# Performance work log

Measured on AMD Instinct MI355X. Metric: run time of the kernel, lower is better.

Reference implementation:

```python
import jax, jax.numpy as jnp
import numpy as np

N, E, G = 100000, 1600000, 1024
F_IN, D, C = 1, 32, 10

def _lin(key, fin, fout):
    return jax.random.normal(key, (fin, fout), jnp.float32) / np.sqrt(fin)

def setup_inputs() -> dict:
    key = jax.random.key(0)
    ks = jax.random.split(key, 32)
    inp = {}
    inp['x'] = jax.random.normal(ks[0], (N, F_IN), jnp.float32)
    inp['edge_index'] = jax.random.randint(ks[1], (2, E), 0, N)
    inp['batch'] = jnp.sort(jax.random.randint(ks[2], (N,), 0, G))
    inp['num_graphs'] = G
    # conv1: ResGatedGraphConv(F_IN -> D)
    inp['c1_Wk'] = _lin(ks[3], F_IN, D); inp['c1_bk'] = jnp.zeros((D,), jnp.float32)
    inp['c1_Wq'] = _lin(ks[4], F_IN, D); inp['c1_bq'] = jnp.zeros((D,), jnp.float32)
    inp['c1_Wv'] = _lin(ks[5], F_IN, D); inp['c1_bv'] = jnp.zeros((D,), jnp.float32)
    inp['c1_Wskip'] = _lin(ks[6], F_IN, D); inp['c1_b'] = jnp.zeros((D,), jnp.float32)
    # conv2: FiLMConv(D -> D), num_relations=1
    inp['c2_Wlin'] = _lin(ks[7], D, D)
    inp['c2_Wfilm'] = _lin(ks[8], D, 2 * D); inp['c2_bfilm'] = jnp.zeros((2 * D,), jnp.float32)
    inp['c2_Wls'] = _lin(ks[9], D, D)
    inp['c2_Wfs'] = _lin(ks[10], D, 2 * D)
    # conv3: ResGatedGraphConv(D -> D)
    inp['c3_Wk'] = _lin(ks[11], D, D); inp['c3_bk'] = jnp.zeros((D,), jnp.float32)
    inp['c3_Wq'] = _lin(ks[12], D, D); inp['c3_bq'] = jnp.zeros((D,), jnp.float32)
    inp['c3_Wv'] = _lin(ks[13], D, D); inp['c3_bv'] = jnp.zeros((D,), jnp.float32)
    inp['c3_Wskip'] = _lin(ks[14], D, D); inp['c3_b'] = jnp.zeros((D,), jnp.float32)
    # final classifier
    inp['lin_W'] = _lin(ks[15], D, C); inp['lin_b'] = jnp.zeros((C,), jnp.float32)
    return inp

def _res_gated(x, src, dst, Wk, bk, Wq, bq, Wv, bv, Wskip, b):
    # out_i = sum_{j->i} sigmoid(k_i + q_j) * v_j + W_skip x_i + b
    k = x @ Wk + bk
    q = x @ Wq + bq
    v = x @ Wv + bv
    msg = jax.nn.sigmoid(k[dst] + q[src]) * v[src]  # [E, D]
    agg = jax.ops.segment_sum(msg, dst, num_segments=x.shape[0])
    return agg + x @ Wskip + b

def _film(x, src, dst, Wlin, Wfilm, bfilm, Wls, Wfs):
    # skip path: relu(gamma_skip * (W_skip x) + beta_skip)
    bg_s = x @ Wfs                       # [N, 2D]
    beta_s, gamma_s = jnp.split(bg_s, 2, axis=-1)
    out = jax.nn.relu(gamma_s * (x @ Wls) + beta_s)
    # message path: relu(gamma_i * (W x_j) + beta_i), mean aggregation
    bg = x @ Wfilm + bfilm
    beta, gamma = jnp.split(bg, 2, axis=-1)
    xl = x @ Wlin
    msg = jax.nn.relu(gamma[dst] * xl[src] + beta[dst])  # [E, D]
    sums = jax.ops.segment_sum(msg, dst, num_segments=x.shape[0])
    cnt = jax.ops.segment_sum(jnp.ones((dst.shape[0], 1), x.dtype), dst, num_segments=x.shape[0])
    return out + sums / jnp.maximum(cnt, 1.0)

def reference(x, edge_index, batch, num_graphs,
              c1_Wk, c1_bk, c1_Wq, c1_bq, c1_Wv, c1_bv, c1_Wskip, c1_b,
              c2_Wlin, c2_Wfilm, c2_bfilm, c2_Wls, c2_Wfs,
              c3_Wk, c3_bk, c3_Wq, c3_bq, c3_Wv, c3_bv, c3_Wskip, c3_b,
              lin_W, lin_b):
    src, dst = edge_index[0], edge_index[1]
    h = _res_gated(x, src, dst, c1_Wk, c1_bk, c1_Wq, c1_bq, c1_Wv, c1_bv, c1_Wskip, c1_b)
    h = jax.nn.relu(h)
    h = _film(h, src, dst, c2_Wlin, c2_Wfilm, c2_bfilm, c2_Wls, c2_Wfs)
    h = jax.nn.relu(h)
    h = _res_gated(h, src, dst, c3_Wk, c3_bk, c3_Wq, c3_bq, c3_Wv, c3_bv, c3_Wskip, c3_b)
    # global mean pool over graphs
    sums = jax.ops.segment_sum(h, batch, num_segments=num_graphs)
    cnt = jax.ops.segment_sum(jnp.ones((h.shape[0], 1), h.dtype), batch, num_segments=num_graphs)
    g = sums / jnp.maximum(cnt, 1.0)
    # dropout is identity in eval mode
    return g @ lin_W + lin_b
```

## Files before the change

### kernel.cpp

```cpp
#include <hip/hip_runtime.h>

#define N_NODES 100000
#define N_EDGES 1600000
#define N_GRAPH 1024
#define NB      196
#define BCAP    10240
#define PEPT    16

typedef unsigned short u16;
typedef unsigned int   u32;

__device__ __forceinline__ u16 f2bf(float f) {
    u32 u = __float_as_uint(f);
    u += 0x7FFFu + ((u >> 16) & 1u);
    return (u16)(u >> 16);
}
__device__ __forceinline__ float bf2f(u16 h) { return __uint_as_float(((u32)h) << 16); }
__device__ __forceinline__ float rcpf(float x) { return __builtin_amdgcn_rcpf(x); }

__global__ __launch_bounds__(256) void k_partition(const int* __restrict__ ei,
                                                   int* __restrict__ gcnt,
                                                   int* __restrict__ bucketed)
{
    __shared__ int lcnt[NB], gbase[NB], lcur[NB];
    int t = threadIdx.x;
    for (int i = t; i < NB; i += 256) { lcnt[i] = 0; lcur[i] = 0; }
    __syncthreads();

    int ebase = blockIdx.x * (256 * PEPT);
    int pk[PEPT], bk[PEPT];
#pragma unroll
    for (int r = 0; r < PEPT; r++) {
        int e = ebase + r * 256 + t;
        if (e < N_EDGES) {
            int d = ei[N_EDGES + e];
            int s = ei[e];
            int b = d >> 9;
            bk[r] = b;
            pk[r] = ((d & 511) << 17) | s;
            atomicAdd(&lcnt[b], 1);
        } else bk[r] = -1;
    }
    __syncthreads();
    for (int i = t; i < NB; i += 256) gbase[i] = atomicAdd(&gcnt[i], lcnt[i]);
    __syncthreads();
#pragma unroll
    for (int r = 0; r < PEPT; r++) {
        if (bk[r] >= 0) {
            int b = bk[r];
            int pos = gbase[b] + atomicAdd(&lcur[b], 1);
            bucketed[b * BCAP + pos] = pk[r];
        }
    }
}

__global__ __launch_bounds__(512) void k_place(const int* __restrict__ bucketed,
                                               const int* __restrict__ gcnt,
                                               int* __restrict__ csr,
                                               int* __restrict__ starts,
                                               int* __restrict__ cnt)
{
    __shared__ int sb[256];
    __shared__ int scnt[512], sexc[512], scur[512];
    int b = blockIdx.x, t = threadIdx.x;

    if (t < 256) sb[t] = (t < NB) ? gcnt[t] : 0;
    __syncthreads();
#pragma unroll
    for (int off = 1; off < 256; off <<= 1) {
        int u = 0;
        if (t < 256 && t >= off) u = sb[t - off];
        __syncthreads();
        if (t < 256) sb[t] += u;
        __syncthreads();
    }
    int ecnt = gcnt[b];
    int ebase = sb[b] - ecnt;
    const int* bp = bucketed + b * BCAP;

    scnt[t] = 0; scur[t] = 0;
    __syncthreads();
    for (int e = t; e < ecnt; e += 512) atomicAdd(&scnt[bp[e] >> 17], 1);
    __syncthreads();
    int v = scnt[t];
    sexc[t] = v;
    __syncthreads();
#pragma unroll
    for (int off = 1; off < 512; off <<= 1) {
        int u = (t >= off) ? sexc[t - off] : 0;
        __syncthreads();
        sexc[t] += u;
        __syncthreads();
    }
    int excl = sexc[t] - v;
    __syncthreads();
    sexc[t] = excl;
    __syncthreads();

    int node = b * 512 + t;
    if (node < N_NODES) { starts[node] = ebase + excl; cnt[node] = v; }

    for (int e = t; e < ecnt; e += 512) {
        int p = bp[e];
        int ld = p >> 17;
        int pos = ebase + sexc[ld] + atomicAdd(&scur[ld], 1);
        csr[pos] = p & 0x1FFFF;
    }
}

#define EDGE1(XS, ACC) {                                                     \
    ACC.x += fmaf(XS, wv.x, bv4.x) *                                         \
             rcpf(fmaf(ek.x, __expf(-fmaf(XS, wq.x, bq4.x)), 1.0f));         \
    ACC.y += fmaf(XS, wv.y, bv4.y) *                                         \
             rcpf(fmaf(ek.y, __expf(-fmaf(XS, wq.y, bq4.y)), 1.0f));         \
    ACC.z += fmaf(XS, wv.z, bv4.z) *                                         \
             rcpf(fmaf(ek.z, __expf(-fmaf(XS, wq.z, bq4.z)), 1.0f));         \
    ACC.w += fmaf(XS, wv.w, bv4.w) *                                         \
             rcpf(fmaf(ek.w, __expf(-fmaf(XS, wq.w, bq4.w)), 1.0f)); }

__global__ __launch_bounds__(256) void k_gath1(
    const float* __restrict__ x, const int* __restrict__ csr_src,
    const int* __restrict__ starts, const int* __restrict__ cnt,
    const float* __restrict__ Wk, const float* __restrict__ bk,
    const float* __restrict__ Wq, const float* __restrict__ bq,
    const float* __restrict__ Wv, const float* __restrict__ bv,
    const float* __restrict__ Wskip, const float* __restrict__ b,
    u16* __restrict__ h1b)
{
    int tid = blockIdx.x * 256 + threadIdx.x;
    int i = tid >> 3, l = tid & 7;

    float xd = x[i];
    float4 wk = ((const float4*)Wk)[l], bk4 = ((const float4*)bk)[l];
    float4 wq = ((const float4*)Wq)[l], bq4 = ((const float4*)bq)[l];
    float4 wv = ((const float4*)Wv)[l], bv4 = ((const float4*)bv)[l];
    float4 ek;
    ek.x = __expf(-fmaf(xd, wk.x, bk4.x));
    ek.y = __expf(-fmaf(xd, wk.y, bk4.y));
    ek.z = __expf(-fmaf(xd, wk.z, bk4.z));
    ek.w = __expf(-fmaf(xd, wk.w, bk4.w));

    int base = starts[i], deg = cnt[i];
    float4 a0 = make_float4(0.f, 0.f, 0.f, 0.f);
    float4 a1 = make_float4(0.f, 0.f, 0.f, 0.f);
    int e = 0;
    for (; e + 3 < deg; e += 4) {
        int s0 = csr_src[base + e];
        int s1 = csr_src[base + e + 1];
        int s2 = csr_src[base + e + 2];
        int s3 = csr_src[base + e + 3];
        float x0 = x[s0], x1 = x[s1], x2 = x[s2], x3 = x[s3];
        EDGE1(x0, a0) EDGE1(x1, a1) EDGE1(x2, a0) EDGE1(x3, a1)
    }
    for (; e < deg; e++) {
        float x0 = x[csr_src[base + e]];
        EDGE1(x0, a0)
    }
    float4 ws4 = ((const float4*)Wskip)[l];
    float4 bb4 = ((const float4*)b)[l];
    ushort4 o;
    o.x = f2bf(a0.x + a1.x + fmaf(xd, ws4.x, bb4.x));
    o.y = f2bf(a0.y + a1.y + fmaf(xd, ws4.y, bb4.y));
    o.z = f2bf(a0.z + a1.z + fmaf(xd, ws4.z, bb4.z));
    o.w = f2bf(a0.w + a1.w + fmaf(xd, ws4.w, bb4.w));
    ((ushort4*)h1b)[(size_t)i * 8 + l] = o;
}

__device__ __forceinline__ float4 dot4(const float* __restrict__ h,
                                       const float* __restrict__ Wcol, int stride)
{
    float4 a = make_float4(0.f, 0.f, 0.f, 0.f);
#pragma unroll
    for (int k = 0; k < 32; k++) {
        float4 w = *(const float4*)(Wcol + k * stride);
        float hk = h[k];
        a.x = fmaf(hk, w.x, a.x);
        a.y = fmaf(hk, w.y, a.y);
        a.z = fmaf(hk, w.z, a.z);
        a.w = fmaf(hk, w.w, a.w);
    }
    return a;
}

__device__ __forceinline__ void load_row_bf16(const u16* __restrict__ rowb,
                                              size_t i, float* h, bool relu)
{
    const uint4* rp = (const uint4*)rowb + i * 4;
#pragma unroll
    for (int j = 0; j < 4; j++) {
        uint4 q = rp[j];
        float v0 = bf2f((u16)q.x), v1 = bf2f((u16)(q.x >> 16));
        float v2 = bf2f((u16)q.y), v3 = bf2f((u16)(q.y >> 16));
        float v4 = bf2f((u16)q.z), v5 = bf2f((u16)(q.z >> 16));
        float v6 = bf2f((u16)q.w), v7 = bf2f((u16)(q.w >> 16));
        if (relu) {
            v0 = fmaxf(v0, 0.f); v1 = fmaxf(v1, 0.f);
            v2 = fmaxf(v2, 0.f); v3 = fmaxf(v3, 0.f);
            v4 = fmaxf(v4, 0.f); v5 = fmaxf(v5, 0.f);
            v6 = fmaxf(v6, 0.f); v7 = fmaxf(v7, 0.f);
        }
        h[8 * j + 0] = v0; h[8 * j + 1] = v1; h[8 * j + 2] = v2; h[8 * j + 3] = v3;
        h[8 * j + 4] = v4; h[8 * j + 5] = v5; h[8 * j + 6] = v6; h[8 * j + 7] = v7;
    }
}

__global__ __launch_bounds__(256) void k_node2(
    const u16* __restrict__ h1b,
    const float* __restrict__ Wlin, const float* __restrict__ Wfilm,
    const float* __restrict__ bfilm, const float* __restrict__ Wls,
    const float* __restrict__ Wfs,
    u16* __restrict__ skip2b, u16* __restrict__ bg2b, u16* __restrict__ xlb)
{
    __shared__ float sWlin[1024], sWfilm[2048], sWls[1024], sWfs[2048];
    int t = threadIdx.x;
    for (int idx = t; idx < 1024; idx += 256) sWlin[idx] = Wlin[idx];
    for (int idx = t; idx < 2048; idx += 256) sWfilm[idx] = Wfilm[idx];
    for (int idx = t; idx < 1024; idx += 256) sWls[idx] = Wls[idx];
    for (int idx = t; idx < 2048; idx += 256) sWfs[idx] = Wfs[idx];
    __syncthreads();

    int tid = blockIdx.x * 256 + t;
    int i = tid >> 3, l = tid & 7;

    float h[32];
    load_row_bf16(h1b, (size_t)i, h, true);

    float4 bs = dot4(h, sWfs + l * 4, 64);
    float4 gs = dot4(h, sWfs + 32 + l * 4, 64);
    float4 ls = dot4(h, sWls + l * 4, 32);
    ushort4 sku;
    sku.x = f2bf(fmaxf(fmaf(gs.x, ls.x, bs.x), 0.f));
    sku.y = f2bf(fmaxf(fmaf(gs.y, ls.y, bs.y), 0.f));
    sku.z = f2bf(fmaxf(fmaf(gs.z, ls.z, bs.z), 0.f));
    sku.w = f2bf(fmaxf(fmaf(gs.w, ls.w, bs.w), 0.f));
    ((ushort4*)skip2b)[(size_t)i * 8 + l] = sku;

    float4 bf0 = ((const float4*)bfilm)[l * 2];
    float4 bf1 = ((const float4*)bfilm)[l * 2 + 1];
    float4 f0 = dot4(h, sWfilm + l * 8, 64);
    float4 f1 = dot4(h, sWfilm + l * 8 + 4, 64);
    f0.x += bf0.x; f0.y += bf0.y; f0.z += bf0.z; f0.w += bf0.w;
    f1.x += bf1.x; f1.y += bf1.y; f1.z += bf1.z; f1.w += bf1.w;
    uint4 pk;
    pk.x = (u32)f2bf(f0.x) | ((u32)f2bf(f0.y) << 16);
    pk.y = (u32)f2bf(f0.z) | ((u32)f2bf(f0.w) << 16);
    pk.z = (u32)f2bf(f1.x) | ((u32)f2bf(f1.y) << 16);
    pk.w = (u32)f2bf(f1.z) | ((u32)f2bf(f1.w) << 16);
    ((uint4*)bg2b)[(size_t)i * 8 + l] = pk;

    float4 xo = dot4(h, sWlin + l * 4, 32);
    ushort4 xp;
    xp.x = f2bf(xo.x); xp.y = f2bf(xo.y); xp.z = f2bf(xo.z); xp.w = f2bf(xo.w);
    ((ushort4*)xlb)[(size_t)i * 8 + l] = xp;
}

#define EDGE_ACC2(U, ACC)                                   \
    ACC.x += fmaxf(fmaf(ga.x, bf2f(U.x), be.x), 0.f);       \
    ACC.y += fmaxf(fmaf(ga.y, bf2f(U.y), be.y), 0.f);       \
    ACC.z += fmaxf(fmaf(ga.z, bf2f(U.z), be.z), 0.f);       \
    ACC.w += fmaxf(fmaf(ga.w, bf2f(U.w), be.w), 0.f);

__global__ __launch_bounds__(256) void k_gath2(
    const int* __restrict__ csr_src, const int* __restrict__ starts,
    const int* __restrict__ cnt,
    const u16* __restrict__ bg2b, const u16* __restrict__ xlb,
    const u16* __restrict__ skip2b, u16* __restrict__ h2b)
{
    int tid = blockIdx.x * 256 + threadIdx.x;
    int i = tid >> 3, l = tid & 7;

    const u16* row = bg2b + (size_t)i * 64;
    ushort4 beu = *(const ushort4*)(row + l * 4);
    ushort4 gau = *(const ushort4*)(row + 32 + l * 4);
    float4 be = make_float4(bf2f(beu.x), bf2f(beu.y), bf2f(beu.z), bf2f(beu.w));
    float4 ga = make_float4(bf2f(gau.x), bf2f(gau.y), bf2f(gau.z), bf2f(gau.w));

    int base = starts[i], deg = cnt[i];
    const ushort4* xp = (const ushort4*)xlb;
    float4 a0 = make_float4(0.f, 0.f, 0.f, 0.f);
    float4 a1 = make_float4(0.f, 0.f, 0.f, 0.f);
    int e = 0;
    for (; e + 7 < deg; e += 8) {
        int s0 = csr_src[base + e];
        int s1 = csr_src[base + e + 1];
        int s2 = csr_src[base + e + 2];
        int s3 = csr_src[base + e + 3];
        int s4 = csr_src[base + e + 4];
        int s5 = csr_src[base + e + 5];
        int s6 = csr_src[base + e + 6];
        int s7 = csr_src[base + e + 7];
        ushort4 u0 = xp[(size_t)s0 * 8 + l];
        ushort4 u1 = xp[(size_t)s1 * 8 + l];
        ushort4 u2 = xp[(size_t)s2 * 8 + l];
        ushort4 u3 = xp[(size_t)s3 * 8 + l];
        ushort4 u4 = xp[(size_t)s4 * 8 + l];
        ushort4 u5 = xp[(size_t)s5 * 8 + l];
        ushort4 u6 = xp[(size_t)s6 * 8 + l];
        ushort4 u7 = xp[(size_t)s7 * 8 + l];
        EDGE_ACC2(u0, a0) EDGE_ACC2(u1, a1) EDGE_ACC2(u2, a0) EDGE_ACC2(u3, a1)
        EDGE_ACC2(u4, a0) EDGE_ACC2(u5, a1) EDGE_ACC2(u6, a0) EDGE_ACC2(u7, a1)
    }
    for (; e < deg; e++) {
        ushort4 u0 = xp[(size_t)csr_src[base + e] * 8 + l];
        EDGE_ACC2(u0, a0)
    }
    float inv = rcpf(fmaxf((float)deg, 1.0f));
    ushort4 sku = ((const ushort4*)skip2b)[(size_t)i * 8 + l];
    ushort4 o;
    o.x = f2bf(fmaxf(fmaf(a0.x + a1.x, inv, bf2f(sku.x)), 0.f));
    o.y = f2bf(fmaxf(fmaf(a0.y + a1.y, inv, bf2f(sku.y)), 0.f));
    o.z = f2bf(fmaxf(fmaf(a0.z + a1.z, inv, bf2f(sku.z)), 0.f));
    o.w = f2bf(fmaxf(fmaf(a0.w + a1.w, inv, bf2f(sku.w)), 0.f));
    ((ushort4*)h2b)[(size_t)i * 8 + l] = o;
}

__global__ __launch_bounds__(256) void k_node3(
    const u16* __restrict__ h2b,
    const float* __restrict__ Wk, const float* __restrict__ bk,
    const float* __restrict__ Wq, const float* __restrict__ bq,
    const float* __restrict__ Wv, const float* __restrict__ bv,
    const float* __restrict__ Wskip, const float* __restrict__ b,
    u16* __restrict__ ek3b, u32* __restrict__ qvb, u16* __restrict__ acc3b)
{
    __shared__ float sWk[1024], sWq[1024], sWv[1024], sWs[1024];
    int t = threadIdx.x;
    for (int idx = t; idx < 1024; idx += 256) {
        sWk[idx] = Wk[idx];
        sWq[idx] = Wq[idx];
        sWv[idx] = Wv[idx];
        sWs[idx] = Wskip[idx];
    }
    __syncthreads();

    int tid = blockIdx.x * 256 + t;
    int i = tid >> 3, l = tid & 7;

    float h[32];
    load_row_bf16(h2b, (size_t)i, h, false);

    float4 bk4 = ((const float4*)bk)[l];
    float4 bq4 = ((const float4*)bq)[l];
    float4 bv4 = ((const float4*)bv)[l];
    float4 bb4 = ((const float4*)b)[l];

    float4 kk = dot4(h, sWk + l * 4, 32);
    ushort4 eku;
    eku.x = f2bf(__expf(-(kk.x + bk4.x)));
    eku.y = f2bf(__expf(-(kk.y + bk4.y)));
    eku.z = f2bf(__expf(-(kk.z + bk4.z)));
    eku.w = f2bf(__expf(-(kk.w + bk4.w)));
    ((ushort4*)ek3b)[(size_t)i * 8 + l] = eku;

    float4 qq = dot4(h, sWq + l * 4, 32);
    float4 vv = dot4(h, sWv + l * 4, 32);
    float eq0 = __expf(-(qq.x + bq4.x));
    float eq1 = __expf(-(qq.y + bq4.y));
    float eq2 = __expf(-(qq.z + bq4.z));
    float eq3 = __expf(-(qq.w + bq4.w));
    vv.x += bv4.x; vv.y += bv4.y; vv.z += bv4.z; vv.w += bv4.w;

    uint4 pk;
    pk.x = (u32)f2bf(eq0) | ((u32)f2bf(eq1) << 16);
    pk.y = (u32)f2bf(eq2) | ((u32)f2bf(eq3) << 16);
    pk.z = (u32)f2bf(vv.x) | ((u32)f2bf(vv.y) << 16);
    pk.w = (u32)f2bf(vv.z) | ((u32)f2bf(vv.w) << 16);
    ((uint4*)qvb)[(size_t)i * 8 + l] = pk;

    float4 ss = dot4(h, sWs + l * 4, 32);
    ushort4 so;
    so.x = f2bf(ss.x + bb4.x);
    so.y = f2bf(ss.y + bb4.y);
    so.z = f2bf(ss.z + bb4.z);
    so.w = f2bf(ss.w + bb4.w);
    ((ushort4*)acc3b)[(size_t)i * 8 + l] = so;
}

#define EDGE_ACC(P, ACC)                                                        \
    ACC.x += bf2f((u16)(P.z)) * rcpf(fmaf(ek.x, bf2f((u16)(P.x)), 1.0f));       \
    ACC.y += bf2f((u16)(P.z >> 16)) * rcpf(fmaf(ek.y, bf2f((u16)(P.x >> 16)), 1.0f)); \
    ACC.z += bf2f((u16)(P.w)) * rcpf(fmaf(ek.z, bf2f((u16)(P.y)), 1.0f));       \
    ACC.w += bf2f((u16)(P.w >> 16)) * rcpf(fmaf(ek.w, bf2f((u16)(P.y >> 16)), 1.0f));

__global__ __launch_bounds__(256) void k_gath3p(
    const int* __restrict__ csr_src, const int* __restrict__ starts,
    const int* __restrict__ cnt,
    const u16* __restrict__ ek3b, const u32* __restrict__ qvb,
    const u16* __restrict__ acc3b, const int* __restrict__ batch,
    float* __restrict__ gsum)
{
    __shared__ float sg[8][32];
    int t = threadIdx.x;
    int tid = blockIdx.x * 256 + t;
    int i = tid >> 3, l = tid & 7;

    sg[t >> 5][t & 31] = 0.f;
    int gmin = batch[blockIdx.x * 32];
    __syncthreads();

    ushort4 eku = ((const ushort4*)ek3b)[(size_t)i * 8 + l];
    float4 ek = make_float4(bf2f(eku.x), bf2f(eku.y), bf2f(eku.z), bf2f(eku.w));
    int base = starts[i], deg = cnt[i];
    const uint4* qv = (const uint4*)qvb;
    float4 a0 = make_float4(0.f, 0.f, 0.f, 0.f);
    float4 a1 = make_float4(0.f, 0.f, 0.f, 0.f);
    int e = 0;
    for (; e + 3 < deg; e += 4) {
        int s0 = csr_src[base + e];
        int s1 = csr_src[base + e + 1];
        int s2 = csr_src[base + e + 2];
        int s3 = csr_src[base + e + 3];
        uint4 p0 = qv[(size_t)s0 * 8 + l];
        uint4 p1 = qv[(size_t)s1 * 8 + l];
        uint4 p2 = qv[(size_t)s2 * 8 + l];
        uint4 p3 = qv[(size_t)s3 * 8 + l];
        EDGE_ACC(p0, a0) EDGE_ACC(p1, a1) EDGE_ACC(p2, a0) EDGE_ACC(p3, a1)
    }
    for (; e < deg; e++) {
        uint4 p0 = qv[(size_t)csr_src[base + e] * 8 + l];
        EDGE_ACC(p0, a0)
    }
    ushort4 sku = ((const ushort4*)acc3b)[(size_t)i * 8 + l];
    float4 o = make_float4(bf2f(sku.x) + a0.x + a1.x, bf2f(sku.y) + a0.y + a1.y,
                           bf2f(sku.z) + a0.z + a1.z, bf2f(sku.w) + a0.w + a1.w);

    int g = batch[i];
    int slot = g - gmin;
    if (slot < 8) {
        atomicAdd(&sg[slot][l * 4 + 0], o.x);
        atomicAdd(&sg[slot][l * 4 + 1], o.y);
        atomicAdd(&sg[slot][l * 4 + 2], o.z);
        atomicAdd(&sg[slot][l * 4 + 3], o.w);
    } else {
        atomicAdd(&gsum[(size_t)g * 32 + l * 4 + 0], o.x);
        atomicAdd(&gsum[(size_t)g * 32 + l * 4 + 1], o.y);
        atomicAdd(&gsum[(size_t)g * 32 + l * 4 + 2], o.z);
        atomicAdd(&gsum[(size_t)g * 32 + l * 4 + 3], o.w);
    }
    __syncthreads();
    int slot2 = t >> 5, feat = t & 31;
    float v = sg[slot2][feat];
    int gout = gmin + slot2;
    if (v != 0.f && gout < N_GRAPH)
        atomicAdd(&gsum[(size_t)gout * 32 + feat], v);
}

__device__ __forceinline__ int lower_bound(const int* __restrict__ a, int key)
{
    int lo = 0, hi = N_NODES;
    while (lo < hi) {
        int mid = (lo + hi) >> 1;
        if (a[mid] < key) lo = mid + 1; else hi = mid;
    }
    return lo;
}

__global__ __launch_bounds__(256) void k_final(
    const float* __restrict__ gsum, const int* __restrict__ batch,
    const float* __restrict__ linW, const float* __restrict__ linb,
    float* __restrict__ out)
{
    int tid = blockIdx.x * 256 + threadIdx.x;
    if (tid >= N_GRAPH * 10) return;
    int g = tid / 10, c = tid % 10;
    int s = lower_bound(batch, g);
    int e = lower_bound(batch, g + 1);
    float inv = rcpf(fmaxf((float)(e - s), 1.0f));
    const float* gr = gsum + (size_t)g * 32;
    float a = 0.f;
#pragma unroll
    for (int k = 0; k < 32; k++) a = fmaf(gr[k], linW[k * 10 + c], a);
    out[tid] = fmaf(a, inv, linb[c]);
}

extern "C" void kernel_launch(void* const* d_in, const int* in_sizes, int n_in,
                              void* d_out, int out_size, void* d_ws, size_t ws_size,
                              hipStream_t stream)
{
    const float* x      = (const float*)d_in[0];
    const int*   ei     = (const int*)d_in[1];
    const int*   batch  = (const int*)d_in[2];
    const float* c1_Wk   = (const float*)d_in[4];
    const float* c1_bk   = (const float*)d_in[5];
    const float* c1_Wq   = (const float*)d_in[6];
    const float* c1_bq   = (const float*)d_in[7];
    const float* c1_Wv   = (const float*)d_in[8];
    const float* c1_bv   = (const float*)d_in[9];
    const float* c1_Wsk  = (const float*)d_in[10];
    const float* c1_b    = (const float*)d_in[11];
    const float* c2_Wlin = (const float*)d_in[12];
    const float* c2_Wfilm= (const float*)d_in[13];
    const float* c2_bfilm= (const float*)d_in[14];
    const float* c2_Wls  = (const float*)d_in[15];
    const float* c2_Wfs  = (const float*)d_in[16];
    const float* c3_Wk   = (const float*)d_in[17];
    const float* c3_bk   = (const float*)d_in[18];
    const float* c3_Wq   = (const float*)d_in[19];
    const float* c3_bq   = (const float*)d_in[20];
    const float* c3_Wv   = (const float*)d_in[21];
    const float* c3_bv   = (const float*)d_in[22];
    const float* c3_Wsk  = (const float*)d_in[23];
    const float* c3_b    = (const float*)d_in[24];
    const float* lin_W   = (const float*)d_in[25];
    const float* lin_b   = (const float*)d_in[26];
    float* out = (float*)d_out;

    const size_t N = N_NODES;

    int*   gcnt    = (int*)d_ws;
    float* gsum    = (float*)(gcnt + 256);
    int*   bucketed= (int*)(gsum + N_GRAPH * 32);
    int*   icsr    = bucketed + NB * BCAP;
    int*   istarts = icsr + N_EDGES;
    int*   icnt    = istarts + N;
    u16*   h1b     = (u16*)(icnt + N);
    u16*   skip2b  = h1b + N * 32;
    u16*   bg2b    = skip2b + N * 32;
    u16*   xlb     = bg2b + N * 64;
    u16*   acc3b   = xlb + N * 32;

    hipMemsetAsync(gcnt, 0, 256 * sizeof(int) + N_GRAPH * 32 * sizeof(float), stream);

    const int TB = 256;
    int gPart  = (N_EDGES + 256 * PEPT - 1) / (256 * PEPT);
    int gNode8 = (N_NODES * 8) / TB;
    int gFin   = (N_GRAPH * 10 + TB - 1) / TB;

    k_partition<<<gPart, TB, 0, stream>>>(ei, gcnt, bucketed);
    k_place<<<NB, 512, 0, stream>>>(bucketed, gcnt, icsr, istarts, icnt);

    k_gath1<<<gNode8, TB, 0, stream>>>(x, icsr, istarts, icnt,
                                       c1_Wk, c1_bk, c1_Wq, c1_bq,
                                       c1_Wv, c1_bv, c1_Wsk, c1_b, h1b);
    k_node2<<<gNode8, TB, 0, stream>>>(h1b, c2_Wlin, c2_Wfilm, c2_bfilm,
                                       c2_Wls, c2_Wfs, skip2b, bg2b, xlb);
    u16* h2b = h1b;
    k_gath2<<<gNode8, TB, 0, stream>>>(icsr, istarts, icnt, bg2b, xlb, skip2b, h2b);
    u16* ek3b = skip2b;
    u32* qvb  = (u32*)bg2b;
    k_node3<<<gNode8, TB, 0, stream>>>(h2b, c3_Wk, c3_bk, c3_Wq, c3_bq,
                                       c3_Wv, c3_bv, c3_Wsk, c3_b,
                                       ek3b, qvb, acc3b);
    k_gath3p<<<gNode8, TB, 0, stream>>>(icsr, istarts, icnt, ek3b, qvb, acc3b,
                                        batch, gsum);
    k_final<<<gFin, TB, 0, stream>>>(gsum, batch, lin_W, lin_b, out);
}
```

Before: 311.2 us.

## Compute FiLM node transforms with bf16 MFMA using prepacked weights

Replaces the scalar per-thread dot products in the conv2 node kernel with 16x16x32 bf16 MFMA instructions, one wave per 16 nodes. A one-block prep kernel packs the four FiLM weight matrices into bf16 fragments in MFMA operand layout. The ReLU after conv1 moves into the gath1 epilogue so the MFMA kernel can read h1 directly. This trades fp32 weights for bf16, which adds rounding error, and the output stores become scattered 2-byte writes instead of vector stores.

Result: faster. 291.5 us (-6.3%).

```diff
diff --git a/kernel.cpp b/kernel.cpp
--- a/kernel.cpp
+++ b/kernel.cpp
@@ -9,6 +9,8 @@
 
 typedef unsigned short u16;
 typedef unsigned int   u32;
+typedef short bf16x8 __attribute__((ext_vector_type(8)));
+typedef float f32x4  __attribute__((ext_vector_type(4)));
 
 __device__ __forceinline__ u16 f2bf(float f) {
     u32 u = __float_as_uint(f);
@@ -17,6 +19,8 @@
 }
 __device__ __forceinline__ float bf2f(u16 h) { return __uint_as_float(((u32)h) << 16); }
 __device__ __forceinline__ float rcpf(float x) { return __builtin_amdgcn_rcpf(x); }
+__device__ __forceinline__ float bflo(u32 p) { return __uint_as_float(p << 16); }
+__device__ __forceinline__ float bfhi(u32 p) { return __uint_as_float(p & 0xFFFF0000u); }
 
 __global__ __launch_bounds__(256) void k_partition(const int* __restrict__ ei,
                                                    int* __restrict__ gcnt,
@@ -159,10 +163,10 @@
     float4 ws4 = ((const float4*)Wskip)[l];
     float4 bb4 = ((const float4*)b)[l];
     ushort4 o;
-    o.x = f2bf(a0.x + a1.x + fmaf(xd, ws4.x, bb4.x));
-    o.y = f2bf(a0.y + a1.y + fmaf(xd, ws4.y, bb4.y));
-    o.z = f2bf(a0.z + a1.z + fmaf(xd, ws4.z, bb4.z));
-    o.w = f2bf(a0.w + a1.w + fmaf(xd, ws4.w, bb4.w));
+    o.x = f2bf(fmaxf(a0.x + a1.x + fmaf(xd, ws4.x, bb4.x), 0.f));
+    o.y = f2bf(fmaxf(a0.y + a1.y + fmaf(xd, ws4.y, bb4.y), 0.f));
+    o.z = f2bf(fmaxf(a0.z + a1.z + fmaf(xd, ws4.z, bb4.z), 0.f));
+    o.w = f2bf(fmaxf(a0.w + a1.w + fmaf(xd, ws4.w, bb4.w), 0.f));
     ((ushort4*)h1b)[(size_t)i * 8 + l] = o;
 }
 
@@ -189,10 +193,10 @@
 #pragma unroll
     for (int j = 0; j < 4; j++) {
         uint4 q = rp[j];
-        float v0 = bf2f((u16)q.x), v1 = bf2f((u16)(q.x >> 16));
-        float v2 = bf2f((u16)q.y), v3 = bf2f((u16)(q.y >> 16));
-        float v4 = bf2f((u16)q.z), v5 = bf2f((u16)(q.z >> 16));
-        float v6 = bf2f((u16)q.w), v7 = bf2f((u16)(q.w >> 16));
+        float v0 = bflo(q.x), v1 = bfhi(q.x);
+        float v2 = bflo(q.y), v3 = bfhi(q.y);
+        float v4 = bflo(q.z), v5 = bfhi(q.z);
+        float v6 = bflo(q.w), v7 = bfhi(q.w);
         if (relu) {
             v0 = fmaxf(v0, 0.f); v1 = fmaxf(v1, 0.f);
             v2 = fmaxf(v2, 0.f); v3 = fmaxf(v3, 0.f);
@@ -204,54 +208,88 @@
     }
 }
 
-__global__ __launch_bounds__(256) void k_node2(
-    const u16* __restrict__ h1b,
+__global__ __launch_bounds__(256) void k_prepw2(
     const float* __restrict__ Wlin, const float* __restrict__ Wfilm,
-    const float* __restrict__ bfilm, const float* __restrict__ Wls,
-    const float* __restrict__ Wfs,
+    const float* __restrict__ Wls, const float* __restrict__ Wfs,
+    u16* __restrict__ wbuf)
+{
+    for (int idx = threadIdx.x; idx < 12 * 512; idx += 256) {
+        int t = idx >> 9, rem = idx & 511;
+        int l = rem >> 3, j = rem & 7;
+        int k = ((l >> 4) << 3) + j, n = l & 15;
+        float v;
+        if      (t < 2)  v = Wls [k * 32 + t * 16 + n];
+        else if (t < 4)  v = Wfs [k * 64 + (t - 2) * 16 + n];
+        else if (t < 6)  v = Wfs [k * 64 + 32 + (t - 4) * 16 + n];
+        else if (t < 8)  v = Wlin[k * 32 + (t - 6) * 16 + n];
+        else if (t < 10) v = Wfilm[k * 64 + (t - 8) * 16 + n];
+        else             v = Wfilm[k * 64 + 32 + (t - 10) * 16 + n];
+        wbuf[idx] = f2bf(v);
+    }
+}
+
+__global__ __launch_bounds__(256) void k_node2m(
+    const u16* __restrict__ h1b, const u16* __restrict__ wbuf,
+    const float* __restrict__ bfilm,
     u16* __restrict__ skip2b, u16* __restrict__ bg2b, u16* __restrict__ xlb)
 {
-    __shared__ float sWlin[1024], sWfilm[2048], sWls[1024], sWfs[2048];
-    int t = threadIdx.x;
-    for (int idx = t; idx < 1024; idx += 256) sWlin[idx] = Wlin[idx];
-    for (int idx = t; idx < 2048; idx += 256) sWfilm[idx] = Wfilm[idx];
-    for (int idx = t; idx < 1024; idx += 256) sWls[idx] = Wls[idx];
-    for (int idx = t; idx < 2048; idx += 256) sWfs[idx] = Wfs[idx];
-    __syncthreads();
-
-    int tid = blockIdx.x * 256 + t;
-    int i = tid >> 3, l = tid & 7;
-
-    float h[32];
-    load_row_bf16(h1b, (size_t)i, h, true);
-
-    float4 bs = dot4(h, sWfs + l * 4, 64);
-    float4 gs = dot4(h, sWfs + 32 + l * 4, 64);
-    float4 ls = dot4(h, sWls + l * 4, 32);
-    ushort4 sku;
-    sku.x = f2bf(fmaxf(fmaf(gs.x, ls.x, bs.x), 0.f));
-    sku.y = f2bf(fmaxf(fmaf(gs.y, ls.y, bs.y), 0.f));
-    sku.z = f2bf(fmaxf(fmaf(gs.z, ls.z, bs.z), 0.f));
-    sku.w = f2bf(fmaxf(fmaf(gs.w, ls.w, bs.w), 0.f));
-    ((ushort4*)skip2b)[(size_t)i * 8 + l] = sku;
-
-    float4 bf0 = ((const float4*)bfilm)[l * 2];
-    float4 bf1 = ((const float4*)bfilm)[l * 2 + 1];
-    float4 f0 = dot4(h, sWfilm + l * 8, 64);
-    float4 f1 = dot4(h, sWfilm + l * 8 + 4, 64);
-    f0.x += bf0.x; f0.y += bf0.y; f0.z += bf0.z; f0.w += bf0.w;
-    f1.x += bf1.x; f1.y += bf1.y; f1.z += bf1.z; f1.w += bf1.w;
-    uint4 pk;
-    pk.x = (u32)f2bf(f0.x) | ((u32)f2bf(f0.y) << 16);
-    pk.y = (u32)f2bf(f0.z) | ((u32)f2bf(f0.w) << 16);
-    pk.z = (u32)f2bf(f1.x) | ((u32)f2bf(f1.y) << 16);
-    pk.w = (u32)f2bf(f1.z) | ((u32)f2bf(f1.w) << 16);
-    ((uint4*)bg2b)[(size_t)i * 8 + l] = pk;
-
-    float4 xo = dot4(h, sWlin + l * 4, 32);
-    ushort4 xp;
-    xp.x = f2bf(xo.x); xp.y = f2bf(xo.y); xp.z = f2bf(xo.z); xp.w = f2bf(xo.w);
-    ((ushort4*)xlb)[(size_t)i * 8 + l] = xp;
+    int lane = threadIdx.x & 63, w = threadIdx.x >> 6;
+    int nb = blockIdx.x * 64 + w * 16;
+    int quad = lane >> 4, c = lane & 15;
+
+    int ia = nb + c;
+    if (ia >= N_NODES) ia = N_NODES - 1;
+    uint4 aq = ((const uint4*)h1b)[(size_t)ia * 4 + quad];
+    bf16x8 a = *(bf16x8*)&aq;
+
+    const uint4* wp = (const uint4*)wbuf;
+    f32x4 z = {0.f, 0.f, 0.f, 0.f};
+
+    uint4 q0 = wp[0 * 64 + lane], q1 = wp[1 * 64 + lane];
+    uint4 q2 = wp[2 * 64 + lane], q3 = wp[3 * 64 + lane];
+    uint4 q4 = wp[4 * 64 + lane], q5 = wp[5 * 64 + lane];
+    f32x4 dls0 = __builtin_amdgcn_mfma_f32_16x16x32_bf16(a, *(bf16x8*)&q0, z, 0, 0, 0);
+    f32x4 dls1 = __builtin_amdgcn_mfma_f32_16x16x32_bf16(a, *(bf16x8*)&q1, z, 0, 0, 0);
+    f32x4 dbs0 = __builtin_amdgcn_mfma_f32_16x16x32_bf16(a, *(bf16x8*)&q2, z, 0, 0, 0);
+    f32x4 dbs1 = __builtin_amdgcn_mfma_f32_16x16x32_bf16(a, *(bf16x8*)&q3, z, 0, 0, 0);
+    f32x4 dgs0 = __builtin_amdgcn_mfma_f32_16x16x32_bf16(a, *(bf16x8*)&q4, z, 0, 0, 0);
+    f32x4 dgs1 = __builtin_amdgcn_mfma_f32_16x16x32_bf16(a, *(bf16x8*)&q5, z, 0, 0, 0);
+#pragma unroll
+    for (int r = 0; r < 4; r++) {
+        int node = nb + quad * 4 + r;
+        if (node < N_NODES) {
+            u16* srow = skip2b + (size_t)node * 32;
+            srow[c]      = f2bf(fmaxf(fmaf(dgs0[r], dls0[r], dbs0[r]), 0.f));
+            srow[16 + c] = f2bf(fmaxf(fmaf(dgs1[r], dls1[r], dbs1[r]), 0.f));
+        }
+    }
+
+    uint4 q6 = wp[6 * 64 + lane], q7 = wp[7 * 64 + lane];
+    uint4 q8 = wp[8 * 64 + lane], q9 = wp[9 * 64 + lane];
+    uint4 qa = wp[10 * 64 + lane], qb = wp[11 * 64 + lane];
+    f32x4 dxl0 = __builtin_amdgcn_mfma_f32_16x16x32_bf16(a, *(bf16x8*)&q6, z, 0, 0, 0);
+    f32x4 dxl1 = __builtin_amdgcn_mfma_f32_16x16x32_bf16(a, *(bf16x8*)&q7, z, 0, 0, 0);
+    f32x4 dbe0 = __builtin_amdgcn_mfma_f32_16x16x32_bf16(a, *(bf16x8*)&q8, z, 0, 0, 0);
+    f32x4 dbe1 = __builtin_amdgcn_mfma_f32_16x16x32_bf16(a, *(bf16x8*)&q9, z, 0, 0, 0);
+    f32x4 dga0 = __builtin_amdgcn_mfma_f32_16x16x32_bf16(a, *(bf16x8*)&qa, z, 0, 0, 0);
+    f32x4 dga1 = __builtin_amdgcn_mfma_f32_16x16x32_bf16(a, *(bf16x8*)&qb, z, 0, 0, 0);
+
+    float bf0 = bfilm[c], bf1 = bfilm[16 + c];
+    float bf2 = bfilm[32 + c], bf3 = bfilm[48 + c];
+#pragma unroll
+    for (int r = 0; r < 4; r++) {
+        int node = nb + quad * 4 + r;
+        if (node < N_NODES) {
+            u16* xrow = xlb + (size_t)node * 32;
+            xrow[c]      = f2bf(dxl0[r]);
+            xrow[16 + c] = f2bf(dxl1[r]);
+            u16* brow = bg2b + (size_t)node * 64;
+            brow[c]      = f2bf(dbe0[r] + bf0);
+            brow[16 + c] = f2bf(dbe1[r] + bf1);
+            brow[32 + c] = f2bf(dga0[r] + bf2);
+            brow[48 + c] = f2bf(dga1[r] + bf3);
+        }
+    }
 }
 
 #define EDGE_ACC2(U, ACC)                                   \
@@ -517,22 +555,24 @@
     u16*   bg2b    = skip2b + N * 32;
     u16*   xlb     = bg2b + N * 64;
     u16*   acc3b   = xlb + N * 32;
+    u16*   wbuf    = acc3b + N * 32;
 
     hipMemsetAsync(gcnt, 0, 256 * sizeof(int) + N_GRAPH * 32 * sizeof(float), stream);
 
     const int TB = 256;
     int gPart  = (N_EDGES + 256 * PEPT - 1) / (256 * PEPT);
     int gNode8 = (N_NODES * 8) / TB;
+    int gN64   = (N_NODES + 63) / 64;
     int gFin   = (N_GRAPH * 10 + TB - 1) / TB;
 
     k_partition<<<gPart, TB, 0, stream>>>(ei, gcnt, bucketed);
+    k_prepw2<<<1, TB, 0, stream>>>(c2_Wlin, c2_Wfilm, c2_Wls, c2_Wfs, wbuf);
     k_place<<<NB, 512, 0, stream>>>(bucketed, gcnt, icsr, istarts, icnt);
 
     k_gath1<<<gNode8, TB, 0, stream>>>(x, icsr, istarts, icnt,
                                        c1_Wk, c1_bk, c1_Wq, c1_bq,
                                        c1_Wv, c1_bv, c1_Wsk, c1_b, h1b);
-    k_node2<<<gNode8, TB, 0, stream>>>(h1b, c2_Wlin, c2_Wfilm, c2_bfilm,
-                                       c2_Wls, c2_Wfs, skip2b, bg2b, xlb);
+    k_node2m<<<gN64, TB, 0, stream>>>(h1b, wbuf, c2_bfilm, skip2b, bg2b, xlb);
     u16* h2b = h1b;
     k_gath2<<<gNode8, TB, 0, stream>>>(icsr, istarts, icnt, bg2b, xlb, skip2b, h2b);
     u16* ek3b = skip2b;
```
